# Kernel optimization log

Hardware: AMD Instinct MI355X
Metric: run time of the kernel (lower is better)

Reference implementation:

```python
import jax, jax.numpy as jnp
import numpy as np

# Module hyperparameters
P_, K_, NH = 8, 4, 8
B, H, W, C = 2, 64, 24, 256


def setup_inputs() -> dict:
    key = jax.random.key(0)
    ks = jax.random.split(key, 16)

    def w(k, shape, s=0.02):
        return (jax.random.normal(k, shape) * s).astype(jnp.float32)

    z = lambda *shape: jnp.zeros(shape, jnp.float32)
    return {
        'x_2d': jax.random.normal(ks[0], (B, H, W, C), dtype=jnp.float32),
        # block projections (used as x @ W + b)
        'wq_proj': w(ks[1], (C, C)), 'bq_proj': z(C),
        'wk_proj': w(ks[2], (C, C)), 'bk_proj': z(C),
        'wv_proj': w(ks[3], (C, C)), 'bv_proj': z(C),
        # routing attention projections
        'wq_a': w(ks[4], (C, C)), 'bq_a': z(C),
        'wk_a': w(ks[5], (C, C)), 'bk_a': z(C),
        'wv_a': w(ks[6], (C, C)), 'bv_a': z(C),
        'wo_a': w(ks[7], (C, C)), 'bo_a': z(C),
        # global conv path (HWIO, 5x5, SAME padding == torch padding=2)
        'conv_w': w(ks[8], (5, 5, C, C)), 'conv_b': z(C),
        # layer norms
        'ln1_g': jnp.ones((C,), jnp.float32), 'ln1_b': z(C),
        'ln2_g': jnp.ones((C,), jnp.float32), 'ln2_b': z(C),
    }


def _layer_norm(t, g, b, eps=1e-5):
    m = t.mean(-1, keepdims=True)
    v = ((t - m) ** 2).mean(-1, keepdims=True)
    return (t - m) / jnp.sqrt(v + eps) * g + b


def reference(x_2d, wq_proj, bq_proj, wk_proj, bk_proj, wv_proj, bv_proj,
              wq_a, bq_a, wk_a, bk_a, wv_a, bv_a, wo_a, bo_a,
              conv_w, conv_b, ln1_g, ln1_b, ln2_g, ln2_b):
    Bb, Hh, Ww, Cc = x_2d.shape
    hp = Hh // P_                      # block height
    dk = Cc // NH
    kv = min(K_, P_)

    x_p = x_2d.reshape(Bb, P_, hp, Ww, Cc)
    q_p = x_p @ wq_proj + bq_proj
    k_p = x_p @ wk_proj + bk_proj
    v_p = x_p @ wv_proj + bv_proj

    # block-level routing: mean-pooled block descriptors -> top-k blocks
    q_loc = q_p.mean((2, 3))           # [B,P,C]
    k_loc = k_p.mean((2, 3))
    S_loc = jnp.einsum('bpc,bqc->bpq', q_loc, k_loc)
    _, R = jax.lax.top_k(S_loc, kv)    # [B,P,kv] int32 indices into P

    # gather routed K/V blocks: [B,P,kv,hp*W,C]
    k_flat = k_p.reshape(Bb, P_, hp * Ww, Cc)
    v_flat = v_p.reshape(Bb, P_, hp * Ww, Cc)
    k_fil = jax.vmap(lambda t, r: t[r])(k_flat, R).reshape(Bb, P_, kv, hp, Ww, Cc)
    v_fil = jax.vmap(lambda t, r: t[r])(v_flat, R).reshape(Bb, P_, kv, hp, Ww, Cc)
    q_un = jnp.broadcast_to(q_p[:, :, None], (Bb, P_, kv, hp, Ww, Cc))

    # multi-head attention over flattened (kv*hp*W) per block p
    L = kv * hp * Ww
    def to_heads(t, w, b):
        t = t @ w + b
        t = t.reshape(Bb, P_, kv, hp, Ww, NH, dk)
        return t.transpose(0, 5, 1, 2, 3, 4, 6).reshape(Bb, NH, P_, L, dk)

    qh = to_heads(q_un, wq_a, bq_a)
    kh = to_heads(k_fil, wk_a, bk_a)
    vh = to_heads(v_fil, wv_a, bv_a)

    scores = jnp.einsum('bhpqd,bhpkd->bhpqk', qh, kh) / jnp.sqrt(jnp.float32(dk))
    attn = jax.nn.softmax(scores, axis=-1)
    ctx = jnp.einsum('bhpqk,bhpkd->bhpqd', attn, vh)
    # 'b h p (k hp w) dk -> b p k hp w (h dk)'
    ctx = ctx.reshape(Bb, NH, P_, kv, hp, Ww, dk).transpose(0, 2, 3, 4, 5, 1, 6)
    ctx = ctx.reshape(Bb, P_, kv, hp, Ww, Cc)
    routing_out = (ctx @ wo_a + bo_a).mean(2)          # [B,P,hp,W,C]

    x_res = _layer_norm(x_p + routing_out, ln1_g, ln1_b)

    # global conv path (NHWC SAME conv, kernel 5)
    kv_g = (k_p + v_p).reshape(Bb, Hh, Ww, Cc)
    g = jax.lax.conv_general_dilated(kv_g, conv_w, (1, 1), 'SAME',
                                     dimension_numbers=('NHWC', 'HWIO', 'NHWC')) + conv_b
    g = g.reshape(Bb, P_, hp, Ww, Cc)

    out = _layer_norm(x_res + g, ln2_g, ln2_b)
    return out.reshape(Bb, Hh, Ww, Cc)
```

## Files before the change

kernel.cpp:

```cpp
#include <hip/hip_runtime.h>
#include <hip/hip_bf16.h>


#define NPOS 3072
#define CD   256
#define NE   (NPOS*CD)

typedef short bf16x8 __attribute__((ext_vector_type(8)));
typedef float f32x4  __attribute__((ext_vector_type(4)));

__device__ inline ushort f2bf(float f) {
    __hip_bfloat16 h = __float2bfloat16(f);
    return *reinterpret_cast<ushort*>(&h);
}
__device__ inline float bf2f(ushort u) {
    unsigned v = ((unsigned)u) << 16;
    return *reinterpret_cast<float*>(&v);
}
__device__ inline bf16x8 addbf(bf16x8 a, bf16x8 b) {
    bf16x8 o;
    #pragma unroll
    for (int j = 0; j < 8; ++j)
        o[j] = (short)f2bf(bf2f((ushort)a[j]) + bf2f((ushort)b[j]));
    return o;
}

__global__ __launch_bounds__(256) void wtransA(
    const float* __restrict__ w0, const float* __restrict__ w1, const float* __restrict__ w2,
    const float* __restrict__ w3, const float* __restrict__ w4, const float* __restrict__ w5,
    const float* __restrict__ w6, const float* __restrict__ cw,
    ushort* __restrict__ wt, ushort* __restrict__ wct, ushort* __restrict__ wstr,
    const float* __restrict__ x,
    const float* __restrict__ bq, const float* __restrict__ bk,
    float* __restrict__ qloc, float* __restrict__ kloc)
{
    __shared__ float l[64*65];
    int blk = blockIdx.x;
    int tid = threadIdx.x;
    if (blk < 512) {
        const float* M;
        ushort* D;
        int r2;
        if (blk < 112) {
            int mat = blk >> 4; r2 = blk & 15;
            M = mat==0?w0:mat==1?w1:mat==2?w2:mat==3?w3:mat==4?w4:mat==5?w5:w6;
            D = wt + (size_t)mat*65536;
        } else {
            int b2 = blk - 112;
            int tap = b2 >> 4; r2 = b2 & 15;
            M = cw + (size_t)tap*65536;
            D = wct + (size_t)tap*65536;
        }
        int ci0 = (r2 >> 2)*64, co0 = (r2 & 3)*64;
        int a = tid >> 6, c = tid & 63;
        #pragma unroll 4
        for (int k = 0; k < 16; ++k) {
            int cil = k*4 + a;
            l[cil*65 + c] = M[(size_t)(ci0 + cil)*256 + co0 + c];
        }
        __syncthreads();
        #pragma unroll 4
        for (int k = 0; k < 16; ++k) {
            int col = k*4 + a;
            D[((size_t)(co0 + col))*256 + ci0 + c] = f2bf(l[c*65 + col]);
        }
    } else if (blk < 524) {
        int b2 = blk - 512;
        int mat = b2 >> 2, quarter = b2 & 3;
        const float* M = mat==0 ? w0 : (mat==1 ? w1 : w2);
        size_t base = (size_t)quarter*16384;
        #pragma unroll
        for (int i = 0; i < 16; ++i) {
            size_t idx = base + (size_t)i*1024 + tid*4;
            float4 v = *(const float4*)(M + idx);
            ushort4 o;
            o.x = f2bf(v.x); o.y = f2bf(v.y); o.z = f2bf(v.z); o.w = f2bf(v.w);
            *(ushort4*)(wstr + (size_t)mat*65536 + idx) = o;
        }
    } else {
        int q2 = blk - 524;
        int bp = q2 & 15, which = q2 >> 4;
        int c = tid;
        float s = 0.f;
        for (int i = 0; i < 192; ++i)
            s += x[((size_t)(bp*192 + i))*256 + c];
        l[c] = s * (1.0f/192.0f);
        __syncthreads();
        const float* W  = which ? w1 : w0;
        const float* Bv = which ? bk : bq;
        float* dst      = which ? kloc : qloc;
        float acc = Bv[c];
        #pragma unroll 8
        for (int k = 0; k < 256; ++k)
            acc += l[k] * W[(size_t)k*256 + c];
        dst[bp*256 + c] = acc;
    }
}

__global__ __launch_bounds__(256) void compose(
    const ushort* __restrict__ wt7, const ushort* __restrict__ wstr,
    const float* __restrict__ bq, const float* __restrict__ bk, const float* __restrict__ bv,
    const float* __restrict__ bqa, const float* __restrict__ bka, const float* __restrict__ bva,
    ushort* __restrict__ wtc, ushort* __restrict__ wtkv, float* __restrict__ bcomp,
    const float* __restrict__ qloc, const float* __restrict__ kloc, int* __restrict__ Rix)
{
    __shared__ __align__(16) ushort As[32*264];
    int y = blockIdx.y;
    int tid = threadIdx.x;
    if (y < 3) {
        const ushort* A = wt7 + (size_t)(3 + y)*65536;
        const ushort* T = wstr + (size_t)y*65536;
        ushort* U = wtc + (size_t)y*65536;
        int m0 = (blockIdx.x >> 1)*32;
        int nh = blockIdx.x & 1;
        #pragma unroll
        for (int i = 0; i < 4; ++i) {
            int c = i*256 + tid;
            int pos = c >> 5, off = (c & 31)*8;
            *(bf16x8*)&As[pos*264 + off] = *(const bf16x8*)(A + (size_t)(m0 + pos)*256 + off);
        }
        __syncthreads();
        int w = tid >> 6, lane = tid & 63, lm = lane & 15, lq = lane >> 4;
        const ushort* tb = T + ((size_t)(nh*128 + w*32 + lm))*256 + lq*8;
        f32x4 acc[2][2];
        #pragma unroll
        for (int mt = 0; mt < 2; ++mt)
            #pragma unroll
            for (int nt = 0; nt < 2; ++nt) acc[mt][nt] = (f32x4){0.f,0.f,0.f,0.f};
        for (int kc = 0; kc < 8; ++kc) {
            bf16x8 bw[2];
            #pragma unroll
            for (int nt = 0; nt < 2; ++nt) bw[nt] = *(const bf16x8*)(tb + nt*4096 + kc*32);
            bf16x8 af[2];
            #pragma unroll
            for (int mt = 0; mt < 2; ++mt)
                af[mt] = *(const bf16x8*)&As[(mt*16 + lm)*264 + kc*32 + lq*8];
            #pragma unroll
            for (int mt = 0; mt < 2; ++mt)
                #pragma unroll
                for (int nt = 0; nt < 2; ++nt)
                    acc[mt][nt] = __builtin_amdgcn_mfma_f32_16x16x32_bf16(af[mt], bw[nt], acc[mt][nt], 0,0,0);
        }
        #pragma unroll
        for (int mt = 0; mt < 2; ++mt)
            #pragma unroll
            for (int nt = 0; nt < 2; ++nt) {
                int n = nh*128 + w*32 + nt*16 + lm;
                #pragma unroll
                for (int j = 0; j < 4; ++j) {
                    int m = m0 + mt*16 + lq*4 + j;
                    U[(size_t)m*256 + n] = f2bf(acc[mt][nt][j]);
                }
            }
    } else if (y == 3) {
        const ushort* wk7 = wt7 + 65536;
        const ushort* wv7 = wt7 + 131072;
        size_t base = (size_t)blockIdx.x*4096 + tid*16;
        #pragma unroll
        for (int i = 0; i < 2; ++i) {
            bf16x8 a = *(const bf16x8*)(wk7 + base + i*8);
            bf16x8 b = *(const bf16x8*)(wv7 + base + i*8);
            *(bf16x8*)(wtkv + base + i*8) = addbf(a, b);
        }
        int bx = blockIdx.x;
        if (bx < 3) {
            const float* bsrc = bx==0 ? bq : (bx==1 ? bk : bv);
            const float* basr = bx==0 ? bqa : (bx==1 ? bka : bva);
            const ushort* wa = wt7 + (size_t)(3 + bx)*65536;
            float s = basr[tid];
            for (int k = 0; k < 256; ++k)
                s += bsrc[k] * bf2f(wa[(size_t)tid*256 + k]);
            bcomp[bx*256 + tid] = s;
        } else if (bx == 3) {
            bcomp[3*256 + tid] = bk[tid] + bv[tid];
        }
    } else {
        if (blockIdx.x >= 2) return;
        float* S = (float*)As;
        int b = blockIdx.x, t = tid;
        if (t < 64) {
            int p = t >> 3, qq = t & 7;
            float s = 0.f;
            for (int c = 0; c < 256; ++c)
                s += qloc[(b*8+p)*256 + c] * kloc[(b*8+qq)*256 + c];
            S[t] = s;
        }
        __syncthreads();
        if (t < 8) {
            float vals[8];
            #pragma unroll
            for (int j = 0; j < 8; ++j) vals[j] = S[t*8 + j];
            for (int j = 0; j < 4; ++j) {
                int best = 0; float bv2 = vals[0];
                #pragma unroll
                for (int i = 1; i < 8; ++i) if (vals[i] > bv2) { bv2 = vals[i]; best = i; }
                Rix[(b*8 + t)*4 + j] = best;
                vals[best] = -1e30f;
            }
        }
    }
}

__global__ __launch_bounds__(256) void gemm_quad(
    const float* __restrict__ A,
    const ushort* __restrict__ wtc, const ushort* __restrict__ wtkv,
    const float* __restrict__ bcomp,
    ushort* __restrict__ U0, ushort* __restrict__ U1,
    ushort* __restrict__ U2, ushort* __restrict__ U3)
{
    __shared__ __align__(16) ushort As[32*264];
    int y = blockIdx.y;
    const ushort* T = (y < 3) ? (wtc + (size_t)y*65536) : wtkv;
    const float* Bi = bcomp + y*256;
    ushort* U = y==0 ? U0 : (y==1 ? U1 : (y==2 ? U2 : U3));
    float sc = (y == 0) ? 0.17677669529663687f : 1.0f;
    int tid = threadIdx.x;
    int m0 = (blockIdx.x >> 1)*32;
    int nh = blockIdx.x & 1;
    #pragma unroll
    for (int i = 0; i < 4; ++i) {
        int c = i*256 + tid;
        int pos = c >> 5, off = (c & 31)*8;
        const float* src = A + (size_t)(m0 + pos)*256 + off;
        float4 v0 = *(const float4*)src;
        float4 v1 = *(const float4*)(src + 4);
        ushort4 o0, o1;
        o0.x = f2bf(v0.x); o0.y = f2bf(v0.y); o0.z = f2bf(v0.z); o0.w = f2bf(v0.w);
        o1.x = f2bf(v1.x); o1.y = f2bf(v1.y); o1.z = f2bf(v1.z); o1.w = f2bf(v1.w);
        *(ushort4*)&As[pos*264 + off]     = o0;
        *(ushort4*)&As[pos*264 + off + 4] = o1;
    }
    __syncthreads();
    int w = tid >> 6, lane = tid & 63, lm = lane & 15, lq = lane >> 4;
    const ushort* tb = T + ((size_t)(nh*128 + w*32 + lm))*256 + lq*8;

    f32x4 acc[2][2];
    #pragma unroll
    for (int mt = 0; mt < 2; ++mt)
        #pragma unroll
        for (int nt = 0; nt < 2; ++nt) acc[mt][nt] = (f32x4){0.f,0.f,0.f,0.f};

    bf16x8 bw[2];
    #pragma unroll
    for (int nt = 0; nt < 2; ++nt) bw[nt] = *(const bf16x8*)(tb + nt*4096);

    for (int kc = 0; kc < 8; ++kc) {
        int nk = (kc + 1 < 8) ? kc + 1 : 7;
        bf16x8 bn[2];
        #pragma unroll
        for (int nt = 0; nt < 2; ++nt) bn[nt] = *(const bf16x8*)(tb + nt*4096 + nk*32);
        bf16x8 af[2];
        #pragma unroll
        for (int mt = 0; mt < 2; ++mt)
            af[mt] = *(const bf16x8*)&As[(mt*16 + lm)*264 + kc*32 + lq*8];
        #pragma unroll
        for (int mt = 0; mt < 2; ++mt)
            #pragma unroll
            for (int nt = 0; nt < 2; ++nt)
                acc[mt][nt] = __builtin_amdgcn_mfma_f32_16x16x32_bf16(af[mt], bw[nt], acc[mt][nt], 0,0,0);
        #pragma unroll
        for (int nt = 0; nt < 2; ++nt) bw[nt] = bn[nt];
    }

    #pragma unroll
    for (int mt = 0; mt < 2; ++mt) {
        #pragma unroll
        for (int nt = 0; nt < 2; ++nt) {
            int n = nh*128 + w*32 + nt*16 + lm;
            float bb = Bi[n];
            #pragma unroll
            for (int j = 0; j < 4; ++j) {
                int m = m0 + mt*16 + lq*4 + j;
                U[(size_t)m*256 + n] = f2bf((acc[mt][nt][j] + bb) * sc);
            }
        }
    }
}

__global__ __launch_bounds__(256) void attn_conv(
    const ushort* __restrict__ qab, const ushort* __restrict__ kab,
    const ushort* __restrict__ vab, const int* __restrict__ Rix,
    float* __restrict__ pl, ushort* __restrict__ pacc,
    const ushort* __restrict__ kvc,
    const ushort* __restrict__ wct, ushort* __restrict__ pconv)
{
    __shared__ __align__(16) ushort SMEM[19008];
    int tid = threadIdx.x;
    int grp = blockIdx.x / 9, rem = blockIdx.x - grp*9;
    if (rem < 5) {
        int cid = grp*5 + rem;
        int ch = cid & 1;
        int t2 = cid >> 1;
        int rp = t2 / 5, dy = t2 - rp*5;
        int b = rp >> 5, y0 = (rp & 31)*2;

        const bf16x8 zero8 = (bf16x8){0,0,0,0,0,0,0,0};
        #pragma unroll
        for (int i = 0; i < 7; ++i) {
            int c = i*256 + tid;
            int row = (c >= 896);
            int cc = c - row*896;
            int pos = cc >> 5, off = (cc & 31)*8;
            int y = y0 + row + dy - 2;
            bf16x8 v = zero8;
            if (y >= 0 && y < 64 && pos >= 2 && pos < 26) {
                size_t sb = ((size_t)((b*64 + y)*24 + (pos - 2)))*256 + off;
                v = *(const bf16x8*)(kvc + sb);
            }
            *(bf16x8*)(&SMEM[row*9504 + pos*264 + off]) = v;
        }
        __syncthreads();

        int w = tid >> 6;
        int lane = tid & 63, lm = lane & 15, lq = lane >> 4;
        const ushort* bbase = wct + ((size_t)((dy*5)*256 + ch*128 + w*32 + lm))*256 + lq*8;
        const ushort* a00 = &SMEM[lm*264 + lq*8];

        f32x4 acc[2][2][2];
        #pragma unroll
        for (int r = 0; r < 2; ++r)
            #pragma unroll
            for (int mt = 0; mt < 2; ++mt)
                #pragma unroll
                for (int nt = 0; nt < 2; ++nt)
                    acc[r][mt][nt] = (f32x4){0.f,0.f,0.f,0.f};

        bf16x8 b0[2], b1[2];
        #pragma unroll
        for (int nt = 0; nt < 2; ++nt) b0[nt] = *(const bf16x8*)(bbase + nt*4096);
        #pragma unroll
        for (int nt = 0; nt < 2; ++nt) b1[nt] = *(const bf16x8*)(bbase + 32 + nt*4096);

        for (int iter = 0; iter < 40; ++iter) {
            int i2 = (iter + 2 < 40) ? iter + 2 : 39;
            int boff = (i2 >> 3)*65536 + (i2 & 7)*32;
            bf16x8 bn[2];
            #pragma unroll
            for (int nt = 0; nt < 2; ++nt) bn[nt] = *(const bf16x8*)(bbase + boff + nt*4096);

            int aoff = (iter >> 3)*264 + (iter & 7)*32;
            bf16x8 af[2][2];
            #pragma unroll
            for (int r = 0; r < 2; ++r)
                #pragma unroll
                for (int mt = 0; mt < 2; ++mt)
                    af[r][mt] = *(const bf16x8*)(a00 + r*9504 + mt*4224 + aoff);

            #pragma unroll
            for (int r = 0; r < 2; ++r)
                #pragma unroll
                for (int mt = 0; mt < 2; ++mt)
                    #pragma unroll
                    for (int nt = 0; nt < 2; ++nt)
                        acc[r][mt][nt] = __builtin_amdgcn_mfma_f32_16x16x32_bf16(
                            af[r][mt], b0[nt], acc[r][mt][nt], 0, 0, 0);

            #pragma unroll
            for (int nt = 0; nt < 2; ++nt) { b0[nt] = b1[nt]; b1[nt] = bn[nt]; }
        }

        #pragma unroll
        for (int r = 0; r < 2; ++r) {
            int grow = rp*2 + r;
            #pragma unroll
            for (int mt = 0; mt < 2; ++mt) {
                #pragma unroll
                for (int nt = 0; nt < 2; ++nt) {
                    int cob = ch*128 + w*32 + nt*16 + lm;
                    #pragma unroll
                    for (int j = 0; j < 4; ++j) {
                        int x = mt*16 + lq*4 + j;
                        if (x < 24)
                            pconv[((size_t)(dy*3072 + grow*24 + x))*256 + cob]
                                = f2bf(acc[r][mt][nt][j]);
                    }
                }
            }
        }
    } else {
        int aid = grp*4 + (rem - 5);
        int bph = aid >> 2, kvb = aid & 3;
        int w = tid >> 6, lane = tid & 63;
        int lm = lane & 15, lq = lane >> 4;
        int bp = bph >> 3, h = bph & 7, b = bp >> 3;
        int r = Rix[bp*4 + kvb];
        int vrow0 = (b*8 + r)*192;
        ushort* P  = SMEM;
        ushort* Vs = SMEM + 2560;

        #pragma unroll
        for (int i = 0; i < 6; ++i) {
            int idx = i*256 + tid;
            int pos = idx >> 3, c4 = (idx & 7)*4;
            ushort4 v = *(const ushort4*)(vab + ((size_t)(vrow0 + pos))*256 + h*32 + c4);
            Vs[(c4+0)*200 + pos] = v.x;
            Vs[(c4+1)*200 + pos] = v.y;
            Vs[(c4+2)*200 + pos] = v.z;
            Vs[(c4+3)*200 + pos] = v.w;
        }

        bf16x8 qf[3];
        #pragma unroll
        for (int t = 0; t < 3; ++t)
            qf[t] = *(const bf16x8*)(qab + ((size_t)(bp*192 + w*48 + t*16 + lm))*256 + h*32 + lq*8);

        const ushort* kbase = kab + ((size_t)(vrow0))*256 + h*32 + lq*8;
        ushort* pw = P + w*640;
        __syncthreads();

        f32x4 O[3][2];
        #pragma unroll
        for (int t = 0; t < 3; ++t) { O[t][0] = (f32x4){0,0,0,0}; O[t][1] = (f32x4){0,0,0,0}; }
        float l[3] = {0.f, 0.f, 0.f};

        for (int k0 = 0; k0 < 192; k0 += 32) {
            bf16x8 kf0 = *(const bf16x8*)(kbase + (size_t)(k0 + lm)*256);
            bf16x8 kf1 = *(const bf16x8*)(kbase + (size_t)(k0 + 16 + lm)*256);
            bf16x8 vf0 = *(const bf16x8*)(&Vs[lm*200 + k0 + lq*8]);
            bf16x8 vf1 = *(const bf16x8*)(&Vs[(16 + lm)*200 + k0 + lq*8]);
            #pragma unroll
            for (int t = 0; t < 3; ++t) {
                f32x4 s0 = __builtin_amdgcn_mfma_f32_16x16x32_bf16(kf0, qf[t], (f32x4){0,0,0,0}, 0,0,0);
                f32x4 s1 = __builtin_amdgcn_mfma_f32_16x16x32_bf16(kf1, qf[t], (f32x4){0,0,0,0}, 0,0,0);
                float p0[4], p1[4];
                #pragma unroll
                for (int j = 0; j < 4; ++j) { p0[j] = __expf(s0[j]); p1[j] = __expf(s1[j]); }
                l[t] += p0[0]+p0[1]+p0[2]+p0[3] + p1[0]+p1[1]+p1[2]+p1[3];
                ushort4 a, c;
                a.x = f2bf(p0[0]); a.y = f2bf(p0[1]); a.z = f2bf(p0[2]); a.w = f2bf(p0[3]);
                c.x = f2bf(p1[0]); c.y = f2bf(p1[1]); c.z = f2bf(p1[2]); c.w = f2bf(p1[3]);
                *(ushort4*)(pw + lm*40 + lq*4)      = a;
                *(ushort4*)(pw + lm*40 + 16 + lq*4) = c;
                bf16x8 pf = *(const bf16x8*)(pw + lm*40 + lq*8);
                O[t][0] = __builtin_amdgcn_mfma_f32_16x16x32_bf16(pf, vf0, O[t][0], 0,0,0);
                O[t][1] = __builtin_amdgcn_mfma_f32_16x16x32_bf16(pf, vf1, O[t][1], 0,0,0);
            }
        }

        #pragma unroll
        for (int t = 0; t < 3; ++t) {
            float lt = l[t];
            lt += __shfl_xor(lt, 16);
            lt += __shfl_xor(lt, 32);
            size_t pbase = ((size_t)(bph*4 + kvb))*192 + w*48 + t*16;
            if (lq == 0) pl[pbase + lm] = lt;
            #pragma unroll
            for (int nt = 0; nt < 2; ++nt)
                #pragma unroll
                for (int reg = 0; reg < 4; ++reg)
                    pacc[(pbase + lq*4 + reg)*32 + nt*16 + lm] = f2bf(O[t][nt][reg]);
        }
    }
}

__global__ __launch_bounds__(256) void gemm_wo_ln2(
    const float* __restrict__ pl, const ushort* __restrict__ pacc,
    const ushort* __restrict__ T, const float* __restrict__ boa,
    const float* __restrict__ x,
    const float* __restrict__ g1, const float* __restrict__ b1,
    const ushort* __restrict__ pc, const float* __restrict__ cb,
    const float* __restrict__ g2, const float* __restrict__ b2,
    float* __restrict__ out)
{
    __shared__ __align__(16) ushort As[16*264];
    __shared__ float L2x[16*256];
    int tid = threadIdx.x;
    int m0 = blockIdx.x*16;
    #pragma unroll
    for (int i = 0; i < 2; ++i) {
        int c = i*256 + tid;
        int pos = c >> 5, off = (c & 31)*8;
        int m = m0 + pos;
        int bp = m / 192, q = m - bp*192;
        int h = off >> 5, d0 = off & 31;
        int bph = bp*8 + h;
        float ls = 0.f;
        float cv[8] = {0,0,0,0,0,0,0,0};
        #pragma unroll
        for (int k = 0; k < 4; ++k) {
            size_t pidx = ((size_t)(bph*4 + k))*192 + q;
            ls += pl[pidx];
            bf16x8 pv = *(const bf16x8*)(pacc + pidx*32 + d0);
            #pragma unroll
            for (int j = 0; j < 8; ++j) cv[j] += bf2f((ushort)pv[j]);
        }
        ushort o[8];
        #pragma unroll
        for (int j = 0; j < 8; ++j) o[j] = f2bf(cv[j] / ls);
        *(ushort4*)&As[pos*264 + off]     = make_ushort4(o[0],o[1],o[2],o[3]);
        *(ushort4*)&As[pos*264 + off + 4] = make_ushort4(o[4],o[5],o[6],o[7]);
    }
    __syncthreads();
    int w = tid >> 6, lane = tid & 63, lm = lane & 15, lq = lane >> 4;
    const ushort* tb = T + ((size_t)(w*64 + lm))*256 + lq*8;

    f32x4 acc[4];
    #pragma unroll
    for (int nt = 0; nt < 4; ++nt) acc[nt] = (f32x4){0.f,0.f,0.f,0.f};

    bf16x8 bw[4];
    #pragma unroll
    for (int nt = 0; nt < 4; ++nt) bw[nt] = *(const bf16x8*)(tb + nt*4096);

    for (int kc = 0; kc < 8; ++kc) {
        int nk = (kc + 1 < 8) ? kc + 1 : 7;
        bf16x8 bn[4];
        #pragma unroll
        for (int nt = 0; nt < 4; ++nt) bn[nt] = *(const bf16x8*)(tb + nt*4096 + nk*32);
        bf16x8 af = *(const bf16x8*)&As[lm*264 + kc*32 + lq*8];
        #pragma unroll
        for (int nt = 0; nt < 4; ++nt)
            acc[nt] = __builtin_amdgcn_mfma_f32_16x16x32_bf16(af, bw[nt], acc[nt], 0,0,0);
        #pragma unroll
        for (int nt = 0; nt < 4; ++nt) bw[nt] = bn[nt];
    }

    #pragma unroll
    for (int nt = 0; nt < 4; ++nt) {
        int n = w*64 + nt*16 + lm;
        float bb = boa[n];
        #pragma unroll
        for (int j = 0; j < 4; ++j) {
            int pos = lq*4 + j;
            float val = acc[nt][j] + bb;
            L2x[pos*256 + n] = val + x[(size_t)(m0 + pos)*256 + n];
        }
    }
    __syncthreads();
    #pragma unroll
    for (int rr = 0; rr < 4; ++rr) {
        int pos = w*4 + rr;
        int grow = m0 + pos;
        float4 a = *(const float4*)(&L2x[pos*256 + lane*4]);
        float x0 = a.x, x1 = a.y, x2 = a.z, x3 = a.w;
        float s  = x0 + x1 + x2 + x3;
        float sq = x0*x0 + x1*x1 + x2*x2 + x3*x3;
        #pragma unroll
        for (int off = 32; off > 0; off >>= 1) {
            s  += __shfl_xor(s,  off);
            sq += __shfl_xor(sq, off);
        }
        float mean = s * (1.0f/256.0f);
        float var  = sq * (1.0f/256.0f) - mean*mean;
        float rstd = rsqrtf(var + 1e-5f);
        float4 gv = *(const float4*)(g1 + lane*4);
        float4 bv = *(const float4*)(b1 + lane*4);
        float r0 = (x0 - mean)*rstd*gv.x + bv.x;
        float r1 = (x1 - mean)*rstd*gv.y + bv.y;
        float r2 = (x2 - mean)*rstd*gv.z + bv.z;
        float r3 = (x3 - mean)*rstd*gv.w + bv.w;
        size_t base = (size_t)grow*256 + lane*4;
        float4 gsum = *(const float4*)(cb + lane*4);
        #pragma unroll
        for (int d = 0; d < 5; ++d) {
            ushort4 v = *(const ushort4*)(pc + (size_t)d*NE + base);
            gsum.x += bf2f(v.x); gsum.y += bf2f(v.y);
            gsum.z += bf2f(v.z); gsum.w += bf2f(v.w);
        }
        float y0 = r0 + gsum.x, y1 = r1 + gsum.y, y2 = r2 + gsum.z, y3 = r3 + gsum.w;
        float s2v  = y0 + y1 + y2 + y3;
        float sq2  = y0*y0 + y1*y1 + y2*y2 + y3*y3;
        #pragma unroll
        for (int off = 32; off > 0; off >>= 1) {
            s2v += __shfl_xor(s2v, off);
            sq2 += __shfl_xor(sq2, off);
        }
        float mean2 = s2v * (1.0f/256.0f);
        float var2  = sq2 * (1.0f/256.0f) - mean2*mean2;
        float rstd2 = rsqrtf(var2 + 1e-5f);
        float4 g2v = *(const float4*)(g2 + lane*4);
        float4 b2v = *(const float4*)(b2 + lane*4);
        float4 o;
        o.x = (y0 - mean2)*rstd2*g2v.x + b2v.x;
        o.y = (y1 - mean2)*rstd2*g2v.y + b2v.y;
        o.z = (y2 - mean2)*rstd2*g2v.z + b2v.z;
        o.w = (y3 - mean2)*rstd2*g2v.w + b2v.w;
        *(float4*)(out + base) = o;
    }
}

extern "C" void kernel_launch(void* const* d_in, const int* in_sizes, int n_in,
                              void* d_out, int out_size, void* d_ws, size_t ws_size,
                              hipStream_t stream)
{
    (void)in_sizes; (void)n_in; (void)out_size; (void)ws_size;
    const float* x    = (const float*)d_in[0];
    const float* wq   = (const float*)d_in[1];
    const float* bq   = (const float*)d_in[2];
    const float* wk   = (const float*)d_in[3];
    const float* bk   = (const float*)d_in[4];
    const float* wv   = (const float*)d_in[5];
    const float* bv   = (const float*)d_in[6];
    const float* wqa  = (const float*)d_in[7];
    const float* bqa  = (const float*)d_in[8];
    const float* wka  = (const float*)d_in[9];
    const float* bka  = (const float*)d_in[10];
    const float* wva  = (const float*)d_in[11];
    const float* bva  = (const float*)d_in[12];
    const float* woa  = (const float*)d_in[13];
    const float* boa  = (const float*)d_in[14];
    const float* cw   = (const float*)d_in[15];
    const float* cbi  = (const float*)d_in[16];
    const float* ln1g = (const float*)d_in[17];
    const float* ln1b = (const float*)d_in[18];
    const float* ln2g = (const float*)d_in[19];
    const float* ln2b = (const float*)d_in[20];
    float* out = (float*)d_out;

    float* ws = (float*)d_ws;
    const size_t HNE = NE/2;
    ushort* qab = (ushort*)(ws + 0*HNE);
    ushort* kab = (ushort*)(ws + 1*HNE);
    ushort* vab = (ushort*)(ws + 2*HNE);
    ushort* kvc = (ushort*)(ws + 3*HNE);
    float* R    = ws + 4*HNE;
    ushort* pacc = (ushort*)R;
    float*  pl   = R + 1572864;
    ushort* pconv= (ushort*)(R + 1671168);
    ushort* wt7  = (ushort*)(R + 3637248);
    ushort* wstr = wt7 + 458752;
    ushort* wtc  = wstr + 196608;
    ushort* wtkv = wtc + 196608;
    ushort* wct  = wtkv + 65536;
    float* bcomp = (float*)(wct + 1638400);
    float* qloc  = bcomp + 1024;
    float* kloc  = qloc + 4096;
    int*   Rix   = (int*)(kloc + 4096);

    wtransA<<<556, 256, 0, stream>>>(wq,wk,wv,wqa,wka,wva,woa, cw, wt7, wct, wstr,
                                     x, bq, bk, qloc, kloc);
    compose<<<dim3(16,5), 256, 0, stream>>>(wt7, wstr, bq,bk,bv, bqa,bka,bva,
                                            wtc, wtkv, bcomp, qloc, kloc, Rix);
    gemm_quad<<<dim3(192,4), 256, 0, stream>>>(x, wtc, wtkv, bcomp, qab, kab, vab, kvc);
    attn_conv<<<1152, 256, 0, stream>>>(qab, kab, vab, Rix, pl, pacc, kvc, wct, pconv);
    gemm_wo_ln2<<<192, 256, 0, stream>>>(pl, pacc, wt7 + 393216, boa, x, ln1g, ln1b,
                                         pconv, cbi, ln2g, ln2b, out);
}
```

Measured before the change: 187.6 us.

## Merge weight transpose and compose kernels into one prep kernel

Measured after the change: 181.2 us. 1.04x faster.

```diff
diff --git a/kernel.cpp b/kernel.cpp
--- a/kernel.cpp
+++ b/kernel.cpp
@@ -17,39 +17,34 @@
     unsigned v = ((unsigned)u) << 16;
     return *reinterpret_cast<float*>(&v);
 }
-__device__ inline bf16x8 addbf(bf16x8 a, bf16x8 b) {
-    bf16x8 o;
-    #pragma unroll
-    for (int j = 0; j < 8; ++j)
-        o[j] = (short)f2bf(bf2f((ushort)a[j]) + bf2f((ushort)b[j]));
-    return o;
-}
-
-__global__ __launch_bounds__(256) void wtransA(
+
+__global__ __launch_bounds__(256) void prep(
     const float* __restrict__ w0, const float* __restrict__ w1, const float* __restrict__ w2,
     const float* __restrict__ w3, const float* __restrict__ w4, const float* __restrict__ w5,
     const float* __restrict__ w6, const float* __restrict__ cw,
-    ushort* __restrict__ wt, ushort* __restrict__ wct, ushort* __restrict__ wstr,
+    ushort* __restrict__ wct, ushort* __restrict__ wwo,
+    ushort* __restrict__ wtc, ushort* __restrict__ wtkv,
     const float* __restrict__ x,
-    const float* __restrict__ bq, const float* __restrict__ bk,
-    float* __restrict__ qloc, float* __restrict__ kloc)
+    const float* __restrict__ bq, const float* __restrict__ bk, const float* __restrict__ bv,
+    const float* __restrict__ bqa, const float* __restrict__ bka, const float* __restrict__ bva,
+    float* __restrict__ bcomp, float* __restrict__ qloc, float* __restrict__ kloc)
 {
-    __shared__ float l[64*65];
+    __shared__ __align__(16) char SM[33280];
     int blk = blockIdx.x;
     int tid = threadIdx.x;
-    if (blk < 512) {
+    if (blk < 416) {
+        float* l = (float*)SM;
         const float* M;
         ushort* D;
         int r2;
-        if (blk < 112) {
-            int mat = blk >> 4; r2 = blk & 15;
-            M = mat==0?w0:mat==1?w1:mat==2?w2:mat==3?w3:mat==4?w4:mat==5?w5:w6;
-            D = wt + (size_t)mat*65536;
-        } else {
-            int b2 = blk - 112;
-            int tap = b2 >> 4; r2 = b2 & 15;
+        if (blk < 400) {
+            int tap = blk >> 4; r2 = blk & 15;
             M = cw + (size_t)tap*65536;
             D = wct + (size_t)tap*65536;
+        } else {
+            r2 = blk - 400;
+            M = w6;
+            D = wwo;
         }
         int ci0 = (r2 >> 2)*64, co0 = (r2 & 3)*64;
         int a = tid >> 6, c = tid & 63;
@@ -64,21 +59,9 @@
             int col = k*4 + a;
             D[((size_t)(co0 + col))*256 + ci0 + c] = f2bf(l[c*65 + col]);
         }
-    } else if (blk < 524) {
-        int b2 = blk - 512;
-        int mat = b2 >> 2, quarter = b2 & 3;
-        const float* M = mat==0 ? w0 : (mat==1 ? w1 : w2);
-        size_t base = (size_t)quarter*16384;
-        #pragma unroll
-        for (int i = 0; i < 16; ++i) {
-            size_t idx = base + (size_t)i*1024 + tid*4;
-            float4 v = *(const float4*)(M + idx);
-            ushort4 o;
-            o.x = f2bf(v.x); o.y = f2bf(v.y); o.z = f2bf(v.z); o.w = f2bf(v.w);
-            *(ushort4*)(wstr + (size_t)mat*65536 + idx) = o;
-        }
-    } else {
-        int q2 = blk - 524;
+    } else if (blk < 448) {
+        float* l = (float*)SM;
+        int q2 = blk - 416;
         int bp = q2 & 15, which = q2 >> 4;
         int c = tid;
         float s = 0.f;
@@ -94,87 +77,123 @@
         for (int k = 0; k < 256; ++k)
             acc += l[k] * W[(size_t)k*256 + c];
         dst[bp*256 + c] = acc;
+    } else if (blk < 452) {
+        int bx = blk - 448;
+        if (bx < 3) {
+            const float* bsrc = bx==0 ? bq : (bx==1 ? bk : bv);
+            const float* basr = bx==0 ? bqa : (bx==1 ? bka : bva);
+            const float* wa   = bx==0 ? w3 : (bx==1 ? w4 : w5);
+            float s = basr[tid];
+            for (int k = 0; k < 256; ++k)
+                s += bsrc[k] * bf2f(f2bf(wa[(size_t)k*256 + tid]));
+            bcomp[bx*256 + tid] = s;
+        } else {
+            bcomp[3*256 + tid] = bk[tid] + bv[tid];
+        }
+    } else if (blk < 500) {
+        int b2 = blk - 452;
+        int mat = b2 >> 4, r2 = b2 & 15;
+        const float* Wa = mat==0 ? w3 : (mat==1 ? w4 : w5);
+        const float* Wx = mat==0 ? w0 : (mat==1 ? w1 : w2);
+        ushort* U = wtc + (size_t)mat*65536;
+        int m0 = (r2 >> 1)*32, nh = r2 & 1;
+        ushort* As = (ushort*)SM;
+        float*  l  = (float*)(SM + 16896);
+        for (int c4 = 0; c4 < 4; ++c4) {
+            int kk0 = c4*64;
+            #pragma unroll
+            for (int i = 0; i < 8; ++i) {
+                int idx = i*256 + tid;
+                int r = idx >> 5, c = idx & 31;
+                l[r*33 + c] = Wa[(size_t)(kk0 + r)*256 + m0 + c];
+            }
+            __syncthreads();
+            #pragma unroll
+            for (int i = 0; i < 8; ++i) {
+                int idx = i*256 + tid;
+                int c = idx >> 6, r = idx & 63;
+                As[c*264 + kk0 + r] = f2bf(l[r*33 + c]);
+            }
+            __syncthreads();
+        }
+        int w = tid >> 6, lane = tid & 63, lm = lane & 15, lq = lane >> 4;
+        const float* tbf = Wx + ((size_t)(nh*128 + w*32 + lm))*256 + lq*8;
+        f32x4 acc[2][2];
+        #pragma unroll
+        for (int mt = 0; mt < 2; ++mt)
+            #pragma unroll
+            for (int nt = 0; nt < 2; ++nt) acc[mt][nt] = (f32x4){0.f,0.f,0.f,0.f};
+        for (int kc = 0; kc < 8; ++kc) {
+            bf16x8 bw[2];
+            #pragma unroll
+            for (int nt = 0; nt < 2; ++nt) {
+                const float* p = tbf + nt*4096 + kc*32;
+                float4 v0 = *(const float4*)p;
+                float4 v1 = *(const float4*)(p + 4);
+                bf16x8 bb;
+                bb[0] = (short)f2bf(v0.x); bb[1] = (short)f2bf(v0.y);
+                bb[2] = (short)f2bf(v0.z); bb[3] = (short)f2bf(v0.w);
+                bb[4] = (short)f2bf(v1.x); bb[5] = (short)f2bf(v1.y);
+                bb[6] = (short)f2bf(v1.z); bb[7] = (short)f2bf(v1.w);
+                bw[nt] = bb;
+            }
+            bf16x8 af[2];
+            #pragma unroll
+            for (int mt = 0; mt < 2; ++mt)
+                af[mt] = *(const bf16x8*)&As[(mt*16 + lm)*264 + kc*32 + lq*8];
+            #pragma unroll
+            for (int mt = 0; mt < 2; ++mt)
+                #pragma unroll
+                for (int nt = 0; nt < 2; ++nt)
+                    acc[mt][nt] = __builtin_amdgcn_mfma_f32_16x16x32_bf16(af[mt], bw[nt], acc[mt][nt], 0,0,0);
+        }
+        #pragma unroll
+        for (int mt = 0; mt < 2; ++mt)
+            #pragma unroll
+            for (int nt = 0; nt < 2; ++nt) {
+                int n = nh*128 + w*32 + nt*16 + lm;
+                #pragma unroll
+                for (int j = 0; j < 4; ++j) {
+                    int m = m0 + mt*16 + lq*4 + j;
+                    U[(size_t)m*256 + n] = f2bf(acc[mt][nt][j]);
+                }
+            }
+    } else {
+        int r2 = blk - 500;
+        int ci0 = (r2 >> 2)*64, co0 = (r2 & 3)*64;
+        float* lk = (float*)SM;
+        float* lv = lk + 64*65;
+        int a = tid >> 6, c = tid & 63;
+        #pragma unroll 4
+        for (int k = 0; k < 16; ++k) {
+            int cil = k*4 + a;
+            size_t idx = (size_t)(ci0 + cil)*256 + co0 + c;
+            lk[cil*65 + c] = w1[idx];
+            lv[cil*65 + c] = w2[idx];
+        }
+        __syncthreads();
+        #pragma unroll 4
+        for (int k = 0; k < 16; ++k) {
+            int col = k*4 + a;
+            ushort ka = f2bf(lk[c*65 + col]);
+            ushort va = f2bf(lv[c*65 + col]);
+            wtkv[((size_t)(co0 + col))*256 + ci0 + c] = f2bf(bf2f(ka) + bf2f(va));
+        }
     }
 }
 
-__global__ __launch_bounds__(256) void compose(
-    const ushort* __restrict__ wt7, const ushort* __restrict__ wstr,
-    const float* __restrict__ bq, const float* __restrict__ bk, const float* __restrict__ bv,
-    const float* __restrict__ bqa, const float* __restrict__ bka, const float* __restrict__ bva,
-    ushort* __restrict__ wtc, ushort* __restrict__ wtkv, float* __restrict__ bcomp,
+__global__ __launch_bounds__(256) void gemm_quad(
+    const float* __restrict__ A,
+    const ushort* __restrict__ wtc, const ushort* __restrict__ wtkv,
+    const float* __restrict__ bcomp,
+    ushort* __restrict__ U0, ushort* __restrict__ U1,
+    ushort* __restrict__ U2, ushort* __restrict__ U3,
     const float* __restrict__ qloc, const float* __restrict__ kloc, int* __restrict__ Rix)
 {
     __shared__ __align__(16) ushort As[32*264];
     int y = blockIdx.y;
     int tid = threadIdx.x;
-    if (y < 3) {
-        const ushort* A = wt7 + (size_t)(3 + y)*65536;
-        const ushort* T = wstr + (size_t)y*65536;
-        ushort* U = wtc + (size_t)y*65536;
-        int m0 = (blockIdx.x >> 1)*32;
-        int nh = blockIdx.x & 1;
-        #pragma unroll
-        for (int i = 0; i < 4; ++i) {
-            int c = i*256 + tid;
-            int pos = c >> 5, off = (c & 31)*8;
-            *(bf16x8*)&As[pos*264 + off] = *(const bf16x8*)(A + (size_t)(m0 + pos)*256 + off);
-        }
-        __syncthreads();
-        int w = tid >> 6, lane = tid & 63, lm = lane & 15, lq = lane >> 4;
-        const ushort* tb = T + ((size_t)(nh*128 + w*32 + lm))*256 + lq*8;
-        f32x4 acc[2][2];
-        #pragma unroll
-        for (int mt = 0; mt < 2; ++mt)
-            #pragma unroll
-            for (int nt = 0; nt < 2; ++nt) acc[mt][nt] = (f32x4){0.f,0.f,0.f,0.f};
-        for (int kc = 0; kc < 8; ++kc) {
-            bf16x8 bw[2];
-            #pragma unroll
-            for (int nt = 0; nt < 2; ++nt) bw[nt] = *(const bf16x8*)(tb + nt*4096 + kc*32);
-            bf16x8 af[2];
-            #pragma unroll
-            for (int mt = 0; mt < 2; ++mt)
-                af[mt] = *(const bf16x8*)&As[(mt*16 + lm)*264 + kc*32 + lq*8];
-            #pragma unroll
-            for (int mt = 0; mt < 2; ++mt)
-                #pragma unroll
-                for (int nt = 0; nt < 2; ++nt)
-                    acc[mt][nt] = __builtin_amdgcn_mfma_f32_16x16x32_bf16(af[mt], bw[nt], acc[mt][nt], 0,0,0);
-        }
-        #pragma unroll
-        for (int mt = 0; mt < 2; ++mt)
-            #pragma unroll
-            for (int nt = 0; nt < 2; ++nt) {
-                int n = nh*128 + w*32 + nt*16 + lm;
-                #pragma unroll
-                for (int j = 0; j < 4; ++j) {
-                    int m = m0 + mt*16 + lq*4 + j;
-                    U[(size_t)m*256 + n] = f2bf(acc[mt][nt][j]);
-                }
-            }
-    } else if (y == 3) {
-        const ushort* wk7 = wt7 + 65536;
-        const ushort* wv7 = wt7 + 131072;
-        size_t base = (size_t)blockIdx.x*4096 + tid*16;
-        #pragma unroll
-        for (int i = 0; i < 2; ++i) {
-            bf16x8 a = *(const bf16x8*)(wk7 + base + i*8);
-            bf16x8 b = *(const bf16x8*)(wv7 + base + i*8);
-            *(bf16x8*)(wtkv + base + i*8) = addbf(a, b);
-        }
-        int bx = blockIdx.x;
-        if (bx < 3) {
-            const float* bsrc = bx==0 ? bq : (bx==1 ? bk : bv);
-            const float* basr = bx==0 ? bqa : (bx==1 ? bka : bva);
-            const ushort* wa = wt7 + (size_t)(3 + bx)*65536;
-            float s = basr[tid];
-            for (int k = 0; k < 256; ++k)
-                s += bsrc[k] * bf2f(wa[(size_t)tid*256 + k]);
-            bcomp[bx*256 + tid] = s;
-        } else if (bx == 3) {
-            bcomp[3*256 + tid] = bk[tid] + bv[tid];
-        }
-    } else {
+    if (y == 4) {
         if (blockIdx.x >= 2) return;
         float* S = (float*)As;
         int b = blockIdx.x, t = tid;
@@ -198,23 +217,12 @@
                 vals[best] = -1e30f;
             }
         }
-    }
-}
-
-__global__ __launch_bounds__(256) void gemm_quad(
-    const float* __restrict__ A,
-    const ushort* __restrict__ wtc, const ushort* __restrict__ wtkv,
-    const float* __restrict__ bcomp,
-    ushort* __restrict__ U0, ushort* __restrict__ U1,
-    ushort* __restrict__ U2, ushort* __restrict__ U3)
-{
-    __shared__ __align__(16) ushort As[32*264];
-    int y = blockIdx.y;
+        return;
+    }
     const ushort* T = (y < 3) ? (wtc + (size_t)y*65536) : wtkv;
     const float* Bi = bcomp + y*256;
     ushort* U = y==0 ? U0 : (y==1 ? U1 : (y==2 ? U2 : U3));
     float sc = (y == 0) ? 0.17677669529663687f : 1.0f;
-    int tid = threadIdx.x;
     int m0 = (blockIdx.x >> 1)*32;
     int nh = blockIdx.x & 1;
     #pragma unroll
@@ -617,9 +625,8 @@
     ushort* pacc = (ushort*)R;
     float*  pl   = R + 1572864;
     ushort* pconv= (ushort*)(R + 1671168);
-    ushort* wt7  = (ushort*)(R + 3637248);
-    ushort* wstr = wt7 + 458752;
-    ushort* wtc  = wstr + 196608;
+    ushort* wwo  = (ushort*)(R + 3637248);
+    ushort* wtc  = wwo + 65536;
     ushort* wtkv = wtc + 196608;
     ushort* wct  = wtkv + 65536;
     float* bcomp = (float*)(wct + 1638400);
@@ -627,12 +634,13 @@
     float* kloc  = qloc + 4096;
     int*   Rix   = (int*)(kloc + 4096);
 
-    wtransA<<<556, 256, 0, stream>>>(wq,wk,wv,wqa,wka,wva,woa, cw, wt7, wct, wstr,
-                                     x, bq, bk, qloc, kloc);
-    compose<<<dim3(16,5), 256, 0, stream>>>(wt7, wstr, bq,bk,bv, bqa,bka,bva,
-                                            wtc, wtkv, bcomp, qloc, kloc, Rix);
-    gemm_quad<<<dim3(192,4), 256, 0, stream>>>(x, wtc, wtkv, bcomp, qab, kab, vab, kvc);
+    prep<<<516, 256, 0, stream>>>(wq,wk,wv,wqa,wka,wva,woa, cw,
+                                  wct, wwo, wtc, wtkv,
+                                  x, bq,bk,bv, bqa,bka,bva,
+                                  bcomp, qloc, kloc);
+    gemm_quad<<<dim3(192,5), 256, 0, stream>>>(x, wtc, wtkv, bcomp,
+                                               qab, kab, vab, kvc, qloc, kloc, Rix);
     attn_conv<<<1152, 256, 0, stream>>>(qab, kab, vab, Rix, pl, pacc, kvc, wct, pconv);
-    gemm_wo_ln2<<<192, 256, 0, stream>>>(pl, pacc, wt7 + 393216, boa, x, ln1g, ln1b,
+    gemm_wo_ln2<<<192, 256, 0, stream>>>(pl, pacc, wwo, boa, x, ln1g, ln1b,
                                          pconv, cbi, ln2g, ln2b, out);
 }
```
